# Kernel tuning notes

Hardware: AMD Instinct MI355X
Metric: run time of the kernel (lower is better)

## Reference

```python
import jax, jax.numpy as jnp
import numpy as np

HIDDEN = 1024
NUM_EXPERTS = 8
TOP_K = 2
BATCH, SEQ = 4, 4096


def setup_inputs() -> dict:
    key = jax.random.key(0)
    ks = jax.random.split(key, 7)
    s = 0.02
    x = jax.random.normal(ks[0], (BATCH, SEQ, HIDDEN), dtype=jnp.float32)
    router_w = jax.random.normal(ks[1], (HIDDEN, NUM_EXPERTS), dtype=jnp.float32) * s
    router_b = jnp.zeros((NUM_EXPERTS,), dtype=jnp.float32)
    w1 = jax.random.normal(ks[2], (NUM_EXPERTS, HIDDEN, 2 * HIDDEN), dtype=jnp.float32) * s
    b1 = jnp.zeros((NUM_EXPERTS, 2 * HIDDEN), dtype=jnp.float32)
    w2 = jax.random.normal(ks[3], (NUM_EXPERTS, 2 * HIDDEN, HIDDEN), dtype=jnp.float32) * s
    b2 = jnp.zeros((NUM_EXPERTS, HIDDEN), dtype=jnp.float32)
    return {"x": x, "router_w": router_w, "router_b": router_b,
            "w1": w1, "b1": b1, "w2": w2, "b2": b2}


def reference(x, router_w, router_b, w1, b1, w2, b2):
    # Router: softmax over experts, then top-k and renormalize.
    logits = jnp.einsum("bsh,he->bse", x, router_w) + router_b        # [B,S,E]
    probs = jax.nn.softmax(logits, axis=-1)
    topk_p, topk_i = jax.lax.top_k(probs, TOP_K)                       # [B,S,K]
    topk_p = topk_p / jnp.sum(topk_p, axis=-1, keepdims=True)

    out = jnp.zeros_like(x)
    for e in range(NUM_EXPERTS):
        # combine weight for this expert (0 for tokens that didn't route here;
        # top_k indices are distinct so at most one slot matches)
        w = jnp.sum(jnp.where(topk_i == e, topk_p, 0.0), axis=-1)      # [B,S]
        h = jax.nn.relu(jnp.einsum("bsh,hf->bsf", x, w1[e]) + b1[e])   # [B,S,2H]
        y = jnp.einsum("bsf,fh->bsh", h, w2[e]) + b2[e]                # [B,S,H]
        out = out + w[..., None] * y
    return out
```

## Files before the change

kernel.cpp:

```cpp
#include <hip/hip_runtime.h>

#define HIDDEN 1024
#define FF 2048
#define NEXP 8
#define NTOK 16384
#define NPAIR (2 * NTOK)
#define MAXT 264

typedef short short8 __attribute__((ext_vector_type(8)));
typedef unsigned short ushort4v __attribute__((ext_vector_type(4)));
typedef float f32x4 __attribute__((ext_vector_type(4)));

__device__ __forceinline__ unsigned short f2b(float f) {
  union { float f; unsigned int u; } v; v.f = f;
  unsigned int u = v.u;
  return (unsigned short)((u + 0x7fffu + ((u >> 16) & 1u)) >> 16);
}

__device__ __forceinline__ void gload16(const unsigned short* g, unsigned short* l) {
  __builtin_amdgcn_global_load_lds(
      (const __attribute__((address_space(1))) unsigned int*)g,
      (__attribute__((address_space(3))) unsigned int*)l,
      16, 0, 0);
}

#define PIPE_WAIT(n) do { \
    asm volatile("s_waitcnt vmcnt(" #n ")" ::: "memory"); \
    __builtin_amdgcn_sched_barrier(0); \
  } while (0)
#define ABAR do { \
    asm volatile("s_barrier" ::: "memory"); \
    __builtin_amdgcn_sched_barrier(0); \
  } while (0)

#define W1T_OFF 0ull
#define W2T_OFF (W1T_OFF + (unsigned long long)NEXP * FF * HIDDEN * 2)
#define H_OFF   (W2T_OFF + (unsigned long long)NEXP * HIDDEN * FF * 2)
#define XB_OFF  (H_OFF + (unsigned long long)NPAIR * FF * 2)
#define CNT_OFF (XB_OFF + (unsigned long long)NTOK * HIDDEN * 2)
#define PLIST_OFF (CNT_OFF + 256ull)
#define PW_OFF    (PLIST_OFF + (unsigned long long)NEXP * NTOK * 4)
#define TOPS_OFF  (PW_OFF + (unsigned long long)NPAIR * 4)
#define W0_OFF    (TOPS_OFF + (unsigned long long)NTOK * 4)
#define WQ_OFF    (W0_OFF + (unsigned long long)NTOK * 4)

__global__ void zero_out_k(float4* __restrict__ out) {
  out[(size_t)blockIdx.x * 256 + threadIdx.x] = float4{0.f, 0.f, 0.f, 0.f};
}

__global__ void zero_cnt_k(int* __restrict__ cnt) {
  if (threadIdx.x < NEXP) cnt[threadIdx.x] = 0;
}

__global__ void transpose_cast_k(const float* __restrict__ in,
                                 unsigned short* __restrict__ out,
                                 int R, int C) {
  __shared__ float tile[32][33];
  const size_t eoff = (size_t)blockIdx.z * R * C;
  const float* inp = in + eoff;
  unsigned short* outp = out + eoff;
  const int c = threadIdx.x & 31;
  const int r0 = threadIdx.x >> 5;
  const int gr = blockIdx.y * 32, gc = blockIdx.x * 32;
#pragma unroll
  for (int i = 0; i < 4; i++) {
    int r = r0 + i * 8;
    tile[r][c] = inp[(size_t)(gr + r) * C + gc + c];
  }
  __syncthreads();
#pragma unroll
  for (int i = 0; i < 4; i++) {
    int r = r0 + i * 8;
    outp[(size_t)(gc + r) * R + gr + c] = f2b(tile[c][r]);
  }
}

__global__ void router_k(const float* __restrict__ x, const float* __restrict__ rw,
                         const float* __restrict__ rb, int* __restrict__ tops,
                         float* __restrict__ w0f, unsigned short* __restrict__ xb) {
  const int wid = threadIdx.x >> 6;
  const int lane = threadIdx.x & 63;
  const int t = blockIdx.x * 4 + wid;
  const float* xr = x + (size_t)t * HIDDEN;
  float acc[8];
#pragma unroll
  for (int e = 0; e < 8; e++) acc[e] = 0.f;
#pragma unroll
  for (int i = 0; i < 16; i++) {
    int hh = lane + 64 * i;
    float xv = xr[hh];
    const float4* rwp = reinterpret_cast<const float4*>(rw + (size_t)hh * 8);
    float4 a = rwp[0], b = rwp[1];
    acc[0] += xv * a.x; acc[1] += xv * a.y; acc[2] += xv * a.z; acc[3] += xv * a.w;
    acc[4] += xv * b.x; acc[5] += xv * b.y; acc[6] += xv * b.z; acc[7] += xv * b.w;
  }
  {
    const float4* xr4 = reinterpret_cast<const float4*>(xr);
    unsigned short* xbr = xb + (size_t)t * HIDDEN;
#pragma unroll
    for (int i = 0; i < 4; i++) {
      float4 f = xr4[lane + 64 * i];
      ushort4v o;
      o[0] = f2b(f.x); o[1] = f2b(f.y); o[2] = f2b(f.z); o[3] = f2b(f.w);
      *reinterpret_cast<ushort4v*>(&xbr[(lane + 64 * i) * 4]) = o;
    }
  }
#pragma unroll
  for (int off = 32; off; off >>= 1) {
#pragma unroll
    for (int e = 0; e < 8; e++) acc[e] += __shfl_xor(acc[e], off);
  }
  if (lane == 0) {
#pragma unroll
    for (int e = 0; e < 8; e++) acc[e] += rb[e];
    int i0 = 0; float m0 = acc[0];
#pragma unroll
    for (int e = 1; e < 8; e++) if (acc[e] > m0) { m0 = acc[e]; i0 = e; }
    int i1 = -1; float m1 = -1e30f;
#pragma unroll
    for (int e = 0; e < 8; e++) if (e != i0 && acc[e] > m1) { m1 = acc[e]; i1 = e; }
    float w0 = 1.f / (1.f + __expf(m1 - m0));
    tops[t] = i0 | (i1 << 4);
    w0f[t] = w0;
  }
}

__global__ __launch_bounds__(256)
void scatter_k(const int* __restrict__ tops, const float* __restrict__ w0f,
               int* __restrict__ cnt, int* __restrict__ plist, float* __restrict__ pw) {
  __shared__ int lcnt[NEXP];
  __shared__ int lbase[NEXP];
  const int tid = threadIdx.x;
  const int t = blockIdx.x * 256 + tid;
  if (tid < NEXP) lcnt[tid] = 0;
  __syncthreads();
  const int packed = tops[t];
  const int i0 = packed & 15, i1 = packed >> 4;
  const float w0 = w0f[t];
  const int s0 = atomicAdd(&lcnt[i0], 1);
  const int s1 = atomicAdd(&lcnt[i1], 1);
  __syncthreads();
  if (tid < NEXP) lbase[tid] = atomicAdd(&cnt[tid], lcnt[tid]);
  __syncthreads();
  plist[i0 * NTOK + lbase[i0] + s0] = 2 * t;
  plist[i1 * NTOK + lbase[i1] + s1] = 2 * t + 1;
  pw[2 * t] = w0;
  pw[2 * t + 1] = 1.f - w0;
}

__global__ void plan_k(const int* __restrict__ cnt, int* __restrict__ workq) {
  if (threadIdx.x == 0) {
    int idx = 0;
    for (int e = 0; e < NEXP; e++) {
      int nt = (cnt[e] + 127) >> 7;
      for (int m = 0; m < nt; m++) workq[idx++] = (e << 16) | m;
    }
    while (idx < MAXT) workq[idx++] = -1;
  }
}

template <int PHASE>
__global__ __launch_bounds__(256, 3)
void ffn_k(const unsigned short* __restrict__ xb, const unsigned short* __restrict__ wT,
           const float* __restrict__ bias, const unsigned short* __restrict__ hin,
           unsigned short* __restrict__ hout, float* __restrict__ out,
           const int* __restrict__ cnt, const int* __restrict__ plist,
           const float* __restrict__ pw, const int* __restrict__ workq) {
  constexpr int K = (PHASE == 1) ? HIDDEN : FF;
  constexpr int N = (PHASE == 1) ? FF : HIDDEN;
  constexpr int NT = K / 32;
  constexpr int NTN = N / 128;
  constexpr int NWG = MAXT * NTN;

  constexpr int q8 = NWG / 8, r8 = NWG % 8;
  const int bid = blockIdx.x;
  const int xcd = bid & 7, idx = bid >> 3;
  const int wgid = (xcd < r8 ? xcd * (q8 + 1) : r8 * (q8 + 1) + (xcd - r8) * q8) + idx;
  const int mt = wgid / NTN;
  const int n0g = (wgid % NTN) * 128;

  const int w = workq[mt];
  if (w < 0) return;
  const int e = w >> 16;
  const int m0g = (w & 0xffff) * 128;
  const int mcnt = cnt[e];
  const int mrem = mcnt - m0g;

  __shared__ alignas(16) unsigned short As[3][128][32];
  __shared__ alignas(16) unsigned short Bs[3][128][32];
  __shared__ int rowpair[128];

  const int tid = threadIdx.x;
  if (tid < 128) rowpair[tid] = (tid < mrem) ? plist[e * NTOK + m0g + tid] : -1;
  __syncthreads();

  const int wid = tid >> 6;
  const int lane = tid & 63;

  const int sslot = (lane & 3) ^ ((lane >> 2) & 3);
  const int rsub = lane >> 2;
  const unsigned short* wTe = wT + (size_t)e * N * K;

  const unsigned short* gA[2];
  const unsigned short* gB[2];
#pragma unroll
  for (int i = 0; i < 2; i++) {
    const int c = wid + i * 4;
    const int row = c * 16 + rsub;
    int p = rowpair[row];
    if (p < 0) p = 0;
    const unsigned short* abase;
    if constexpr (PHASE == 1) abase = xb + (size_t)(p >> 1) * HIDDEN;
    else                      abase = hin + (size_t)p * FF;
    gA[i] = abase + sslot * 8;
    gB[i] = wTe + (size_t)(n0g + row) * K + sslot * 8;
  }

  const int wr = (wid >> 1) * 64;
  const int wc = (wid & 1) * 64;
  const int fr = lane & 15;
  const int fg = lane >> 4;
  const int fsw = (fr & 3);

  f32x4 acc[4][4];
#pragma unroll
  for (int i = 0; i < 4; i++)
#pragma unroll
    for (int j = 0; j < 4; j++) acc[i][j] = f32x4{0.f, 0.f, 0.f, 0.f};

#pragma unroll
  for (int b = 0; b < 3; b++) {
#pragma unroll
    for (int i = 0; i < 2; i++) {
      const int c = wid + i * 4;
      gload16(gA[i] + b * 32, &As[b][c * 16][0]);
      gload16(gB[i] + b * 32, &Bs[b][c * 16][0]);
    }
  }

  int cur = 0;
  for (int t = 0; t < NT; ++t) {
    if (t < NT - 2)       PIPE_WAIT(8);
    else if (t == NT - 2) PIPE_WAIT(4);
    else                  PIPE_WAIT(0);
    ABAR;

    short8 af[4], bf[4];
#pragma unroll
    for (int mi = 0; mi < 4; mi++)
      af[mi] = *(const short8*)&As[cur][wr + mi * 16 + fr][(fg ^ fsw) * 8];
#pragma unroll
    for (int ni = 0; ni < 4; ni++)
      bf[ni] = *(const short8*)&Bs[cur][wc + ni * 16 + fr][(fg ^ fsw) * 8];
#pragma unroll
    for (int mi = 0; mi < 4; mi++)
#pragma unroll
      for (int ni = 0; ni < 4; ni++)
        acc[mi][ni] = __builtin_amdgcn_mfma_f32_16x16x32_bf16(af[mi], bf[ni], acc[mi][ni], 0, 0, 0);

    ABAR;

    if (t + 3 < NT) {
      const int kt = (t + 3) * 32;
#pragma unroll
      for (int i = 0; i < 2; i++) {
        const int c = wid + i * 4;
        gload16(gA[i] + kt, &As[cur][c * 16][0]);
        gload16(gB[i] + kt, &Bs[cur][c * 16][0]);
      }
    }
    cur = (cur == 2) ? 0 : cur + 1;
  }

  float bv[4];
#pragma unroll
  for (int ni = 0; ni < 4; ni++) bv[ni] = bias[(size_t)e * N + n0g + wc + ni * 16 + fr];

#pragma unroll
  for (int mi = 0; mi < 4; mi++) {
#pragma unroll
    for (int r = 0; r < 4; r++) {
      int m = wr + mi * 16 + fg * 4 + r;
      if (m >= mrem) continue;
      int p = rowpair[m];
      if constexpr (PHASE == 1) {
        unsigned short* hr = hout + (size_t)p * FF + n0g;
#pragma unroll
        for (int ni = 0; ni < 4; ni++) {
          float v = acc[mi][ni][r] + bv[ni];
          hr[wc + ni * 16 + fr] = f2b(fmaxf(v, 0.f));
        }
      } else {
        float wgt = pw[p];
        float* orow = out + (size_t)(p >> 1) * HIDDEN + n0g;
#pragma unroll
        for (int ni = 0; ni < 4; ni++) {
          float v = (acc[mi][ni][r] + bv[ni]) * wgt;
          atomicAdd(&orow[wc + ni * 16 + fr], v);
        }
      }
    }
  }
}

extern "C" void kernel_launch(void* const* d_in, const int* in_sizes, int n_in,
                              void* d_out, int out_size, void* d_ws, size_t ws_size,
                              hipStream_t stream) {
  const float* x  = (const float*)d_in[0];
  const float* rw = (const float*)d_in[1];
  const float* rb = (const float*)d_in[2];
  const float* w1 = (const float*)d_in[3];
  const float* b1 = (const float*)d_in[4];
  const float* w2 = (const float*)d_in[5];
  const float* b2 = (const float*)d_in[6];
  float* out = (float*)d_out;
  char* ws = (char*)d_ws;

  unsigned short* w1t = (unsigned short*)(ws + W1T_OFF);
  unsigned short* w2t = (unsigned short*)(ws + W2T_OFF);
  unsigned short* h   = (unsigned short*)(ws + H_OFF);
  unsigned short* xb  = (unsigned short*)(ws + XB_OFF);
  int* cnt   = (int*)(ws + CNT_OFF);
  int* plist = (int*)(ws + PLIST_OFF);
  float* pwt = (float*)(ws + PW_OFF);
  int* tops  = (int*)(ws + TOPS_OFF);
  float* w0f = (float*)(ws + W0_OFF);
  int* workq = (int*)(ws + WQ_OFF);

  hipLaunchKernelGGL(zero_cnt_k, dim3(1), dim3(64), 0, stream, cnt);
  hipLaunchKernelGGL(zero_out_k, dim3(16384), dim3(256), 0, stream, (float4*)out);
  hipLaunchKernelGGL(transpose_cast_k, dim3(FF / 32, HIDDEN / 32, NEXP), dim3(256), 0, stream,
                     w1, w1t, HIDDEN, FF);
  hipLaunchKernelGGL(transpose_cast_k, dim3(HIDDEN / 32, FF / 32, NEXP), dim3(256), 0, stream,
                     w2, w2t, FF, HIDDEN);
  hipLaunchKernelGGL(router_k, dim3(NTOK / 4), dim3(256), 0, stream, x, rw, rb, tops, w0f, xb);
  hipLaunchKernelGGL(scatter_k, dim3(NTOK / 256), dim3(256), 0, stream, tops, w0f, cnt, plist, pwt);
  hipLaunchKernelGGL(plan_k, dim3(1), dim3(64), 0, stream, cnt, workq);
  hipLaunchKernelGGL(ffn_k<1>, dim3(MAXT * (FF / 128)), dim3(256), 0, stream,
                     xb, w1t, b1, (const unsigned short*)nullptr, h, (float*)nullptr,
                     cnt, plist, pwt, workq);
  hipLaunchKernelGGL(ffn_k<2>, dim3(MAXT * (HIDDEN / 128)), dim3(256), 0, stream,
                     xb, w2t, b2, h, (unsigned short*)nullptr, out,
                     cnt, plist, pwt, workq);
}
```

Baseline: 540.0 us.

## Switch FFN GEMM to 64-wide K tiles with double buffering and setprio

Each K step of the expert FFN GEMM now covers 64 elements instead of 32. The shared-memory pipeline goes from three buffers to two, and the XOR swizzle is changed to an 8-slot pattern. It adds s_setprio around the MFMA block and lowers the launch-bounds occupancy hint from 3 to 2 blocks per CU. The goal is to halve the barrier and wait overhead per K element while keeping LDS accesses conflict-free, at the cost of less prefetch depth and lower occupancy.

Measured after the change: 568.9 us. +5.4%, slower.

```diff
diff --git a/kernel.cpp b/kernel.cpp
--- a/kernel.cpp
+++ b/kernel.cpp
@@ -160,7 +160,7 @@
 }
 
 template <int PHASE>
-__global__ __launch_bounds__(256, 3)
+__global__ __launch_bounds__(256, 2)
 void ffn_k(const unsigned short* __restrict__ xb, const unsigned short* __restrict__ wT,
            const float* __restrict__ bias, const unsigned short* __restrict__ hin,
            unsigned short* __restrict__ hout, float* __restrict__ out,
@@ -168,7 +168,7 @@
            const float* __restrict__ pw, const int* __restrict__ workq) {
   constexpr int K = (PHASE == 1) ? HIDDEN : FF;
   constexpr int N = (PHASE == 1) ? FF : HIDDEN;
-  constexpr int NT = K / 32;
+  constexpr int NT = K / 64;
   constexpr int NTN = N / 128;
   constexpr int NWG = MAXT * NTN;
 
@@ -186,8 +186,8 @@
   const int mcnt = cnt[e];
   const int mrem = mcnt - m0g;
 
-  __shared__ alignas(16) unsigned short As[3][128][32];
-  __shared__ alignas(16) unsigned short Bs[3][128][32];
+  __shared__ alignas(16) unsigned short As[2][128][64];
+  __shared__ alignas(16) unsigned short Bs[2][128][64];
   __shared__ int rowpair[128];
 
   const int tid = threadIdx.x;
@@ -197,30 +197,29 @@
   const int wid = tid >> 6;
   const int lane = tid & 63;
 
-  const int sslot = (lane & 3) ^ ((lane >> 2) & 3);
-  const int rsub = lane >> 2;
+  const int lrow = lane >> 3;
+  const int gcol = ((lane & 7) ^ lrow) * 8;
   const unsigned short* wTe = wT + (size_t)e * N * K;
 
-  const unsigned short* gA[2];
-  const unsigned short* gB[2];
-#pragma unroll
-  for (int i = 0; i < 2; i++) {
-    const int c = wid + i * 4;
-    const int row = c * 16 + rsub;
-    int p = rowpair[row];
+  const unsigned short* gA[4];
+  const unsigned short* gB[4];
+#pragma unroll
+  for (int j = 0; j < 4; j++) {
+    const int r = wid * 32 + j * 8 + lrow;
+    int p = rowpair[r];
     if (p < 0) p = 0;
     const unsigned short* abase;
     if constexpr (PHASE == 1) abase = xb + (size_t)(p >> 1) * HIDDEN;
     else                      abase = hin + (size_t)p * FF;
-    gA[i] = abase + sslot * 8;
-    gB[i] = wTe + (size_t)(n0g + row) * K + sslot * 8;
+    gA[j] = abase + gcol;
+    gB[j] = wTe + (size_t)(n0g + r) * K + gcol;
   }
 
   const int wr = (wid >> 1) * 64;
   const int wc = (wid & 1) * 64;
   const int fr = lane & 15;
   const int fg = lane >> 4;
-  const int fsw = (fr & 3);
+  const int fr7 = fr & 7;
 
   f32x4 acc[4][4];
 #pragma unroll
@@ -229,47 +228,50 @@
     for (int j = 0; j < 4; j++) acc[i][j] = f32x4{0.f, 0.f, 0.f, 0.f};
 
 #pragma unroll
-  for (int b = 0; b < 3; b++) {
-#pragma unroll
-    for (int i = 0; i < 2; i++) {
-      const int c = wid + i * 4;
-      gload16(gA[i] + b * 32, &As[b][c * 16][0]);
-      gload16(gB[i] + b * 32, &Bs[b][c * 16][0]);
-    }
-  }
-
-  int cur = 0;
+  for (int j = 0; j < 4; j++) {
+    gload16(gA[j], &As[0][wid * 32 + j * 8][0]);
+    gload16(gB[j], &Bs[0][wid * 32 + j * 8][0]);
+  }
+#pragma unroll
+  for (int j = 0; j < 4; j++) {
+    gload16(gA[j] + 64, &As[1][wid * 32 + j * 8][0]);
+    gload16(gB[j] + 64, &Bs[1][wid * 32 + j * 8][0]);
+  }
+
   for (int t = 0; t < NT; ++t) {
-    if (t < NT - 2)       PIPE_WAIT(8);
-    else if (t == NT - 2) PIPE_WAIT(4);
-    else                  PIPE_WAIT(0);
+    const int c = t & 1;
+    if (t + 1 < NT) PIPE_WAIT(8);
+    else            PIPE_WAIT(0);
     ABAR;
 
-    short8 af[4], bf[4];
-#pragma unroll
-    for (int mi = 0; mi < 4; mi++)
-      af[mi] = *(const short8*)&As[cur][wr + mi * 16 + fr][(fg ^ fsw) * 8];
-#pragma unroll
-    for (int ni = 0; ni < 4; ni++)
-      bf[ni] = *(const short8*)&Bs[cur][wc + ni * 16 + fr][(fg ^ fsw) * 8];
-#pragma unroll
-    for (int mi = 0; mi < 4; mi++)
+#pragma unroll
+    for (int kk = 0; kk < 2; kk++) {
+      short8 af[4], bf[4];
+#pragma unroll
+      for (int mi = 0; mi < 4; mi++)
+        af[mi] = *(const short8*)&As[c][wr + mi * 16 + fr][((kk * 4 + fg) ^ fr7) * 8];
 #pragma unroll
       for (int ni = 0; ni < 4; ni++)
-        acc[mi][ni] = __builtin_amdgcn_mfma_f32_16x16x32_bf16(af[mi], bf[ni], acc[mi][ni], 0, 0, 0);
+        bf[ni] = *(const short8*)&Bs[c][wc + ni * 16 + fr][((kk * 4 + fg) ^ fr7) * 8];
+      __builtin_amdgcn_s_setprio(1);
+#pragma unroll
+      for (int mi = 0; mi < 4; mi++)
+#pragma unroll
+        for (int ni = 0; ni < 4; ni++)
+          acc[mi][ni] = __builtin_amdgcn_mfma_f32_16x16x32_bf16(af[mi], bf[ni], acc[mi][ni], 0, 0, 0);
+      __builtin_amdgcn_s_setprio(0);
+    }
 
     ABAR;
 
-    if (t + 3 < NT) {
-      const int kt = (t + 3) * 32;
-#pragma unroll
-      for (int i = 0; i < 2; i++) {
-        const int c = wid + i * 4;
-        gload16(gA[i] + kt, &As[cur][c * 16][0]);
-        gload16(gB[i] + kt, &Bs[cur][c * 16][0]);
+    if (t + 2 < NT) {
+      const int kt = (t + 2) * 64;
+#pragma unroll
+      for (int j = 0; j < 4; j++) {
+        gload16(gA[j] + kt, &As[c][wid * 32 + j * 8][0]);
+        gload16(gB[j] + kt, &Bs[c][wid * 32 + j * 8][0]);
       }
     }
-    cur = (cur == 2) ? 0 : cur + 1;
   }
 
   float bv[4];
```

## Replace atomic scatter-add in second GEMM with bf16 per-pair buffer and combine kernel

Applied to the files above, without the earlier changes.

When the workspace is large enough, the second expert GEMM writes each routed pair's output as bf16 into a per-pair buffer instead of atomically adding weighted fp32 values into the output. A separate combine kernel then reads both pair rows per token and writes the weighted sum directly, so the output zero-fill is dropped. This targets the cost of scattered fp32 atomics and the zeroing pass. In exchange it adds a 64 MB bf16 intermediate write and read, and the output is rounded to bf16 before combining.

Result: no change. 540.4 us (+0.1%).

```diff
diff --git a/kernel.cpp b/kernel.cpp
--- a/kernel.cpp
+++ b/kernel.cpp
@@ -15,6 +15,10 @@
   union { float f; unsigned int u; } v; v.f = f;
   unsigned int u = v.u;
   return (unsigned short)((u + 0x7fffu + ((u >> 16) & 1u)) >> 16);
+}
+__device__ __forceinline__ float b2f(unsigned short b) {
+  union { unsigned int u; float f; } v; v.u = ((unsigned int)b) << 16;
+  return v.f;
 }
 
 __device__ __forceinline__ void gload16(const unsigned short* g, unsigned short* l) {
@@ -43,6 +47,8 @@
 #define TOPS_OFF  (PW_OFF + (unsigned long long)NPAIR * 4)
 #define W0_OFF    (TOPS_OFF + (unsigned long long)NTOK * 4)
 #define WQ_OFF    (W0_OFF + (unsigned long long)NTOK * 4)
+#define YP_OFF    (WQ_OFF + 4096ull)
+#define WS_NEED   (YP_OFF + (unsigned long long)NPAIR * HIDDEN * 2)
 
 __global__ void zero_out_k(float4* __restrict__ out) {
   out[(size_t)blockIdx.x * 256 + threadIdx.x] = float4{0.f, 0.f, 0.f, 0.f};
@@ -159,7 +165,21 @@
   }
 }
 
-template <int PHASE>
+__global__ __launch_bounds__(256)
+void combine_k(const unsigned short* __restrict__ ypair, const float* __restrict__ pw,
+               float* __restrict__ out) {
+  const int t = blockIdx.x * 2 + (threadIdx.x >> 7);
+  const int i = (threadIdx.x & 127) * 8;
+  const float w0 = pw[2 * t], w1 = pw[2 * t + 1];
+  const short8 y0 = *(const short8*)&ypair[(size_t)(2 * t) * HIDDEN + i];
+  const short8 y1 = *(const short8*)&ypair[(size_t)(2 * t + 1) * HIDDEN + i];
+  float* orow = out + (size_t)t * HIDDEN + i;
+#pragma unroll
+  for (int j = 0; j < 8; j++)
+    orow[j] = w0 * b2f((unsigned short)y0[j]) + w1 * b2f((unsigned short)y1[j]);
+}
+
+template <int PHASE, int YP>
 __global__ __launch_bounds__(256, 3)
 void ffn_k(const unsigned short* __restrict__ xb, const unsigned short* __restrict__ wT,
            const float* __restrict__ bias, const unsigned short* __restrict__ hin,
@@ -289,6 +309,13 @@
         for (int ni = 0; ni < 4; ni++) {
           float v = acc[mi][ni][r] + bv[ni];
           hr[wc + ni * 16 + fr] = f2b(fmaxf(v, 0.f));
+        }
+      } else if constexpr (YP == 1) {
+        unsigned short* yr = hout + (size_t)p * HIDDEN + n0g;
+#pragma unroll
+        for (int ni = 0; ni < 4; ni++) {
+          float v = acc[mi][ni][r] + bv[ni];
+          yr[wc + ni * 16 + fr] = f2b(v);
         }
       } else {
         float wgt = pw[p];
@@ -326,9 +353,13 @@
   int* tops  = (int*)(ws + TOPS_OFF);
   float* w0f = (float*)(ws + W0_OFF);
   int* workq = (int*)(ws + WQ_OFF);
+  unsigned short* ypair = (unsigned short*)(ws + YP_OFF);
+
+  const bool use_yp = (ws_size >= WS_NEED);
 
   hipLaunchKernelGGL(zero_cnt_k, dim3(1), dim3(64), 0, stream, cnt);
-  hipLaunchKernelGGL(zero_out_k, dim3(16384), dim3(256), 0, stream, (float4*)out);
+  if (!use_yp)
+    hipLaunchKernelGGL(zero_out_k, dim3(16384), dim3(256), 0, stream, (float4*)out);
   hipLaunchKernelGGL(transpose_cast_k, dim3(FF / 32, HIDDEN / 32, NEXP), dim3(256), 0, stream,
                      w1, w1t, HIDDEN, FF);
   hipLaunchKernelGGL(transpose_cast_k, dim3(HIDDEN / 32, FF / 32, NEXP), dim3(256), 0, stream,
@@ -336,10 +367,17 @@
   hipLaunchKernelGGL(router_k, dim3(NTOK / 4), dim3(256), 0, stream, x, rw, rb, tops, w0f, xb);
   hipLaunchKernelGGL(scatter_k, dim3(NTOK / 256), dim3(256), 0, stream, tops, w0f, cnt, plist, pwt);
   hipLaunchKernelGGL(plan_k, dim3(1), dim3(64), 0, stream, cnt, workq);
-  hipLaunchKernelGGL(ffn_k<1>, dim3(MAXT * (FF / 128)), dim3(256), 0, stream,
+  hipLaunchKernelGGL((ffn_k<1, 0>), dim3(MAXT * (FF / 128)), dim3(256), 0, stream,
                      xb, w1t, b1, (const unsigned short*)nullptr, h, (float*)nullptr,
                      cnt, plist, pwt, workq);
-  hipLaunchKernelGGL(ffn_k<2>, dim3(MAXT * (HIDDEN / 128)), dim3(256), 0, stream,
-                     xb, w2t, b2, h, (unsigned short*)nullptr, out,
-                     cnt, plist, pwt, workq);
-}
+  if (use_yp) {
+    hipLaunchKernelGGL((ffn_k<2, 1>), dim3(MAXT * (HIDDEN / 128)), dim3(256), 0, stream,
+                       xb, w2t, b2, h, ypair, (float*)nullptr,
+                       cnt, plist, pwt, workq);
+    hipLaunchKernelGGL(combine_k, dim3(NTOK / 2), dim3(256), 0, stream, ypair, pwt, out);
+  } else {
+    hipLaunchKernelGGL((ffn_k<2, 0>), dim3(MAXT * (HIDDEN / 128)), dim3(256), 0, stream,
+                       xb, w2t, b2, h, (unsigned short*)nullptr, out,
+                       cnt, plist, pwt, workq);
+  }
+}
```
